# Performance work log

Measured on AMD Instinct MI355X. Metric: run time of the kernel, lower is better.

The kernel has to match this reference:

```python
import jax, jax.numpy as jnp
import numpy as np

N_NODES = 100000
N_EDGES = 1600000


def _mean_agg(x, src, dst, n):
    # mean over incoming neighbors: scatter-add gathered features, divide by degree
    agg = jax.ops.segment_sum(x[src], dst, num_segments=n)  # [N, d]
    deg = jax.ops.segment_sum(jnp.ones((src.shape[0],), x.dtype), dst, num_segments=n)
    return agg / jnp.maximum(deg, 1.0)[:, None]


def _sage_conv(x, src, dst, Wl, Wr, b):
    # PyG SAGEConv (aggr='mean', root_weight=True): lin_l(mean_agg) + lin_r(x) + bias
    n = x.shape[0]
    agg = _mean_agg(x, src, dst, n)
    return agg @ Wl + x @ Wr + b


def setup_inputs() -> dict:
    key = jax.random.key(0)
    ks = jax.random.split(key, 12)
    d_in, d_h, d_out = 128, 256, 47
    x = jax.random.normal(ks[0], (N_NODES, d_in), dtype=jnp.float32)
    src = jax.random.randint(ks[1], (N_EDGES,), 0, N_NODES, dtype=jnp.int32)
    dst = jax.random.randint(ks[2], (N_EDGES,), 0, N_NODES, dtype=jnp.int32)

    def glorot(k, shape):
        lim = 1.0 / np.sqrt(shape[0])
        return jax.random.uniform(k, shape, jnp.float32, -lim, lim)

    return {
        "x": x, "src": src, "dst": dst,
        "Wl0": glorot(ks[3], (d_in, d_h)), "Wr0": glorot(ks[4], (d_in, d_h)), "b0": jnp.zeros((d_h,), jnp.float32),
        "Wl1": glorot(ks[5], (d_h, d_h)), "Wr1": glorot(ks[6], (d_h, d_h)), "b1": jnp.zeros((d_h,), jnp.float32),
        "Wl2": glorot(ks[7], (d_h, d_out)), "Wr2": glorot(ks[8], (d_h, d_out)), "b2": jnp.zeros((d_out,), jnp.float32),
    }


def reference(x, src, dst, Wl0, Wr0, b0, Wl1, Wr1, b1, Wl2, Wr2, b2):
    # layer 1 + ReLU (dropout inactive at inference)
    h = jax.nn.relu(_sage_conv(x, src, dst, Wl0, Wr0, b0))
    # layer 2 + ReLU
    h = jax.nn.relu(_sage_conv(h, src, dst, Wl1, Wr1, b1))
    # output layer + log_softmax
    h = _sage_conv(h, src, dst, Wl2, Wr2, b2)
    return jax.nn.log_softmax(h, axis=-1)
```

## Files before the change

### kernel.cpp

```cpp
#include <hip/hip_runtime.h>
#include <stdint.h>

typedef unsigned int u32;
typedef unsigned short u16;

typedef __attribute__((ext_vector_type(4))) float f32x4;
typedef __attribute__((ext_vector_type(8))) __bf16 bf16x8;

#define NN 100000
#define NE 1600000
#define NSLICE 8
#define SLICE_NODES 12500

typedef __attribute__((address_space(1))) u32 ga_u32;
typedef __attribute__((address_space(3))) u32 ls_u32;

static __device__ __forceinline__ u32 f2bf_bits(float f){
  u32 u = __float_as_uint(f);
  return (u + 0x7fffu + ((u >> 16) & 1u)) >> 16;
}
static __device__ __forceinline__ float bf2f(u16 h){ return __uint_as_float(((u32)h) << 16); }

static __device__ __forceinline__ void gload16(const void* g, void* l){
  __builtin_amdgcn_global_load_lds((const ga_u32*)g, (ls_u32*)l, 16, 0, 0);
}

__global__ void k_hist(const int* __restrict__ dst, int* __restrict__ cnt){
  int e = blockIdx.x*256 + threadIdx.x;
  if (e < NE) atomicAdd(&cnt[dst[e]], 1);
}

__global__ void k_scan1(const int* __restrict__ cnt, int* __restrict__ excl, int* __restrict__ bsum){
  __shared__ int s[1024];
  int t = threadIdx.x;
  int i = blockIdx.x*1024 + t;
  int v = (i < NN) ? cnt[i] : 0;
  s[t] = v; __syncthreads();
  int acc = v;
  for (int off = 1; off < 1024; off <<= 1){
    int tmp = (t >= off) ? s[t-off] : 0;
    __syncthreads();
    acc += tmp; s[t] = acc;
    __syncthreads();
  }
  if (i < NN) excl[i] = acc - v;
  if (t == 1023) bsum[blockIdx.x] = acc;
}

__global__ void k_scan2(int* bsum, int nb){
  if (threadIdx.x == 0 && blockIdx.x == 0){
    int run = 0;
    for (int b = 0; b < nb; b++){ int t = bsum[b]; bsum[b] = run; run += t; }
  }
}

__global__ void k_scan3(const int* __restrict__ cnt, int* __restrict__ row_start,
                        const int* __restrict__ bsum, int* __restrict__ fill_ptr,
                        float* __restrict__ rdeg){
  int i = blockIdx.x*256 + threadIdx.x;
  if (i >= NN) return;
  int rs = row_start[i] + bsum[i >> 10];
  row_start[i] = rs;
  fill_ptr[i]  = rs;
  int c = cnt[i];
  rdeg[i] = 1.0f / (float)(c > 1 ? c : 1);
}

__global__ __launch_bounds__(256) void k_fill(const int* __restrict__ src,
    const int* __restrict__ dst, int* __restrict__ fill_ptr, int* __restrict__ ssrc){
  int slice = blockIdx.x & 7;
  int bin   = blockIdx.x >> 3;
  int nbin  = gridDim.x >> 3;
  int lo = slice * SLICE_NODES;
  int hi = lo + SLICE_NODES;
  for (int e = bin*256 + threadIdx.x; e < NE; e += nbin*256){
    int d = dst[e];
    if (d >= lo && d < hi){
      int pos = atomicAdd(&fill_ptr[d], 1);
      ssrc[pos] = src[e];
    }
  }
}

__global__ void k_wprep(const float* __restrict__ Wl0, const float* __restrict__ Wr0,
                        const float* __restrict__ Wl1, const float* __restrict__ Wr1,
                        const float* __restrict__ Wl2, const float* __restrict__ Wr2,
                        u16* __restrict__ W1t, u16* __restrict__ W2t, u16* __restrict__ W3t){
  int idx = blockIdx.x*256 + threadIdx.x;
  if (idx < 256*256){
    int n = idx >> 8, k = idx & 255;
    float v = (k < 128) ? Wl0[k*256 + n] : Wr0[(k-128)*256 + n];
    W1t[idx] = (u16)f2bf_bits(v);
  } else if (idx < 256*256 + 256*512){
    int j = idx - 256*256;
    int n = j >> 9, k = j & 511;
    float v = (k < 256) ? Wl1[k*256 + n] : Wr1[(k-256)*256 + n];
    W2t[j] = (u16)f2bf_bits(v);
  } else {
    int j = idx - (256*256 + 256*512);
    int n = j >> 8, k = j & 255;
    float v = 0.f;
    if (n < 47) v = Wl2[k*47 + n];
    else if (n >= 48 && n < 95) v = Wr2[k*47 + (n-48)];
    W3t[j] = (u16)f2bf_bits(v);
  }
}

__global__ void k_xconv(const float* __restrict__ x, u16* __restrict__ xb){
  int i = blockIdx.x*256 + threadIdx.x;
  if (i >= NN*128/4) return;
  const float4* xp = (const float4*)x;
  float4 v = xp[i];
  u32 lo = f2bf_bits(v.x) | (f2bf_bits(v.y) << 16);
  u32 hi = f2bf_bits(v.z) | (f2bf_bits(v.w) << 16);
  ((u32*)xb)[2*i]   = lo;
  ((u32*)xb)[2*i+1] = hi;
}

template<int F, int UN>
__global__ __launch_bounds__(256) void k_agg(const u16* __restrict__ feat,
    const int* __restrict__ row_start, const int* __restrict__ cnt,
    const float* __restrict__ rdeg, const int* __restrict__ ssrc,
    u16* __restrict__ out){
  constexpr int EPL = F/64;
  int i = blockIdx.x*4 + (threadIdx.x >> 6);
  if (i >= NN) return;
  int lane = threadIdx.x & 63;
  const u16* fp = feat + (size_t)lane*EPL;
  int beg = row_start[i], num = cnt[i];
  float a0=0.f, b0=0.f, a1=0.f, b1=0.f;
  int j = 0;
  for (; j + UN <= num; j += UN){
    u32 w0[UN], w1[UN];
    #pragma unroll
    for (int u = 0; u < UN; u++){
      const u16* q = fp + (size_t)ssrc[beg+j+u]*F;
      if constexpr (EPL == 4){ uint2 t2 = *(const uint2*)q; w0[u] = t2.x; w1[u] = t2.y; }
      else                   { w0[u] = *(const u32*)q; }
    }
    #pragma unroll
    for (int u = 0; u < UN; u++){
      a0 += __uint_as_float(w0[u] << 16); b0 += __uint_as_float(w0[u] & 0xffff0000u);
      if constexpr (EPL == 4){
        a1 += __uint_as_float(w1[u] << 16); b1 += __uint_as_float(w1[u] & 0xffff0000u);
      }
    }
  }
  for (; j + 2 <= num; j += 2){
    u32 w0[2], w1[2];
    #pragma unroll
    for (int u = 0; u < 2; u++){
      const u16* q = fp + (size_t)ssrc[beg+j+u]*F;
      if constexpr (EPL == 4){ uint2 t2 = *(const uint2*)q; w0[u] = t2.x; w1[u] = t2.y; }
      else                   { w0[u] = *(const u32*)q; }
    }
    #pragma unroll
    for (int u = 0; u < 2; u++){
      a0 += __uint_as_float(w0[u] << 16); b0 += __uint_as_float(w0[u] & 0xffff0000u);
      if constexpr (EPL == 4){
        a1 += __uint_as_float(w1[u] << 16); b1 += __uint_as_float(w1[u] & 0xffff0000u);
      }
    }
  }
  if (j < num){
    const u16* q = fp + (size_t)ssrc[beg+j]*F;
    if constexpr (EPL == 4){
      uint2 t2 = *(const uint2*)q;
      a0 += __uint_as_float(t2.x << 16); b0 += __uint_as_float(t2.x & 0xffff0000u);
      a1 += __uint_as_float(t2.y << 16); b1 += __uint_as_float(t2.y & 0xffff0000u);
    } else {
      u32 p = *(const u32*)q;
      a0 += __uint_as_float(p << 16); b0 += __uint_as_float(p & 0xffff0000u);
    }
  }
  float r = rdeg[i];
  if constexpr (EPL == 4){
    uint2 pk;
    pk.x = f2bf_bits(a0*r) | (f2bf_bits(b0*r) << 16);
    pk.y = f2bf_bits(a1*r) | (f2bf_bits(b1*r) << 16);
    *(uint2*)(out + (size_t)i*F + lane*4) = pk;
  } else {
    *(u32*)(out + (size_t)i*F + lane*2) = f2bf_bits(a0*r) | (f2bf_bits(b0*r) << 16);
  }
}

template<bool RELU>
__global__ __launch_bounds__(256) void k_gemm(
    const u16* __restrict__ A1, int K1, const u16* __restrict__ A2, int K2,
    const u16* __restrict__ Bt, const float* __restrict__ bias,
    u16* __restrict__ C, int ldc){
  __shared__ u16 As[128*64];
  __shared__ u16 Bs[128*64];
  const int M = NN;
  const int K = K1 + K2;
  const int gm = (M + 127) >> 7;
  int bm = blockIdx.x % gm, bn = blockIdx.x / gm;
  int tid = threadIdx.x;
  int lane = tid & 63, w = tid >> 6;
  int wm = w >> 1, wn = w & 1;
  int lr = lane & 15, l4 = lane >> 4;
  f32x4 acc[4][4] = {};
  const int nk = K >> 6;
  for (int kstep = 0; kstep < nk; kstep++){
    __syncthreads();
    #pragma unroll
    for (int q = 0; q < 4; q++){
      int L = q*4096 + tid*16;
      int row = L >> 7;
      int c16 = ((L >> 4) & 7) ^ (row & 7);
      int gk = (kstep << 6) + (c16 << 3);
      int grow = bm*128 + row; if (grow >= M) grow = M - 1;
      const u16* ga = (gk < K1) ? (A1 + (size_t)grow*K1 + gk)
                                : (A2 + (size_t)grow*K2 + (gk - K1));
      gload16(ga, (char*)As + L);
      int gcol = bn*128 + row;
      gload16(Bt + (size_t)gcol*K + gk, (char*)Bs + L);
    }
    __syncthreads();
    #pragma unroll
    for (int kk = 0; kk < 2; kk++){
      bf16x8 af[4], bf[4];
      #pragma unroll
      for (int fm = 0; fm < 4; fm++){
        int row = wm*64 + fm*16 + lr;
        int c16 = (kk << 2) + l4;
        af[fm] = *(const bf16x8*)((const char*)As + row*128 + ((c16 ^ (row&7)) << 4));
      }
      #pragma unroll
      for (int fn = 0; fn < 4; fn++){
        int row = wn*64 + fn*16 + lr;
        int c16 = (kk << 2) + l4;
        bf[fn] = *(const bf16x8*)((const char*)Bs + row*128 + ((c16 ^ (row&7)) << 4));
      }
      #pragma unroll
      for (int fm = 0; fm < 4; fm++)
        #pragma unroll
        for (int fn = 0; fn < 4; fn++)
          acc[fm][fn] = __builtin_amdgcn_mfma_f32_16x16x32_bf16(af[fm], bf[fn], acc[fm][fn], 0, 0, 0);
    }
  }
  #pragma unroll
  for (int fn = 0; fn < 4; fn++){
    int col = bn*128 + wn*64 + fn*16 + lr;
    float bv = bias ? bias[col] : 0.f;
    #pragma unroll
    for (int fm = 0; fm < 4; fm++){
      #pragma unroll
      for (int q = 0; q < 4; q++){
        int rowg = bm*128 + wm*64 + fm*16 + l4*4 + q;
        if (rowg < M){
          float v = acc[fm][fn][q] + bv;
          if (RELU) v = fmaxf(v, 0.f);
          C[(size_t)rowg*ldc + col] = (u16)f2bf_bits(v);
        }
      }
    }
  }
}

__global__ __launch_bounds__(256) void k_final(const u16* __restrict__ G,
    const int* __restrict__ row_start, const int* __restrict__ cnt,
    const float* __restrict__ rdeg, const int* __restrict__ ssrc,
    const float* __restrict__ b2, float* __restrict__ out){
  int i = blockIdx.x*8 + (threadIdx.x >> 5);
  if (i >= NN) return;
  int t = threadIdx.x & 31;
  int beg = row_start[i], num = cnt[i];
  const u16* gp = G + 2*t;
  float a = 0.f, b = 0.f;
  int j = 0;
  for (; j + 4 <= num; j += 4){
    u32 w[4];
    #pragma unroll
    for (int u = 0; u < 4; u++) w[u] = *(const u32*)(gp + (size_t)ssrc[beg+j+u]*128);
    #pragma unroll
    for (int u = 0; u < 4; u++){ a += __uint_as_float(w[u] << 16); b += __uint_as_float(w[u] & 0xffff0000u); }
  }
  for (; j < num; j++){
    u32 w = *(const u32*)(gp + (size_t)ssrc[beg+j]*128);
    a += __uint_as_float(w << 16); b += __uint_as_float(w & 0xffff0000u);
  }
  float r = rdeg[i];
  u32 rw = *(const u32*)(G + (size_t)i*128 + 48 + 2*t);
  int f0 = 2*t, f1 = 2*t + 1;
  float va = (f0 < 47) ? a*r + __uint_as_float(rw << 16)          + b2[f0] : -3.0e38f;
  float vb = (f1 < 47) ? b*r + __uint_as_float(rw & 0xffff0000u)  + b2[f1] : -3.0e38f;
  float m = fmaxf(va, vb);
  #pragma unroll
  for (int o = 16; o > 0; o >>= 1) m = fmaxf(m, __shfl_xor(m, o, 32));
  float e = 0.f;
  if (f0 < 47) e += expf(va - m);
  if (f1 < 47) e += expf(vb - m);
  float s = e;
  #pragma unroll
  for (int o = 16; o > 0; o >>= 1) s += __shfl_xor(s, o, 32);
  float ls = logf(s);
  if (f0 < 47) out[(size_t)i*47 + f0] = va - m - ls;
  if (f1 < 47) out[(size_t)i*47 + f1] = vb - m - ls;
}

extern "C" void kernel_launch(void* const* d_in, const int* in_sizes, int n_in,
                              void* d_out, int out_size, void* d_ws, size_t ws_size,
                              hipStream_t stream){
  const float* x   = (const float*)d_in[0];
  const int*   src = (const int*)d_in[1];
  const int*   dst = (const int*)d_in[2];
  const float* Wl0 = (const float*)d_in[3];
  const float* Wr0 = (const float*)d_in[4];
  const float* b0  = (const float*)d_in[5];
  const float* Wl1 = (const float*)d_in[6];
  const float* Wr1 = (const float*)d_in[7];
  const float* b1  = (const float*)d_in[8];
  const float* Wl2 = (const float*)d_in[9];
  const float* Wr2 = (const float*)d_in[10];
  const float* b2  = (const float*)d_in[11];
  float* out = (float*)d_out;

  char* p = (char*)d_ws;
  size_t off = 0;
  auto alloc = [&](size_t bytes)->char*{
    char* r = p + off; off += (bytes + 511) & ~((size_t)511); return r;
  };
  int*   cnt       = (int*)  alloc((size_t)NN*4);
  int*   row_start = (int*)  alloc((size_t)NN*4);
  int*   fill_ptr  = (int*)  alloc((size_t)NN*4);
  float* rdeg      = (float*)alloc((size_t)NN*4);
  int*   bsum      = (int*)  alloc(512);
  int*   ssrc      = (int*)  alloc((size_t)NE*4);
  u16*   W1t       = (u16*)  alloc((size_t)256*256*2);
  u16*   W2t       = (u16*)  alloc((size_t)256*512*2);
  u16*   W3t       = (u16*)  alloc((size_t)128*256*2);
  u16*   xb        = (u16*)  alloc((size_t)NN*128*2);
  u16*   agg1      = (u16*)  alloc((size_t)NN*128*2);
  u16*   h1        = (u16*)  alloc((size_t)NN*256*2);
  u16*   agg2      = (u16*)  alloc((size_t)NN*256*2);
  u16*   h2        = (u16*)  alloc((size_t)NN*256*2);
  u16*   G = xb;

  const int nb_scan = (NN + 1023) / 1024;

  hipMemsetAsync(cnt, 0, (size_t)NN*4, stream);
  k_hist <<<NE/256, 256, 0, stream>>>(dst, cnt);
  k_scan1<<<nb_scan, 1024, 0, stream>>>(cnt, row_start, bsum);
  k_scan2<<<1, 64, 0, stream>>>(bsum, nb_scan);
  k_scan3<<<(NN+255)/256, 256, 0, stream>>>(cnt, row_start, bsum, fill_ptr, rdeg);
  k_fill <<<8*784, 256, 0, stream>>>(src, dst, fill_ptr, ssrc);
  k_wprep<<<(256*256 + 256*512 + 128*256)/256, 256, 0, stream>>>(Wl0,Wr0,Wl1,Wr1,Wl2,Wr2,W1t,W2t,W3t);
  k_xconv<<<(NN*128/4 + 255)/256, 256, 0, stream>>>(x, xb);

  k_agg<128,16><<<(NN+3)/4, 256, 0, stream>>>(xb, row_start, cnt, rdeg, ssrc, agg1);
  k_gemm<true><<<782*2, 256, 0, stream>>>(agg1, 128, xb, 128, W1t, b0, h1, 256);

  k_agg<256,8><<<(NN+3)/4, 256, 0, stream>>>(h1, row_start, cnt, rdeg, ssrc, agg2);
  k_gemm<true><<<782*2, 256, 0, stream>>>(agg2, 256, h1, 256, W2t, b1, h2, 256);

  k_gemm<false><<<782, 256, 0, stream>>>(h2, 256, h2, 0, W3t, nullptr, G, 128);
  k_final<<<(NN+7)/8, 256, 0, stream>>>(G, row_start, cnt, rdeg, ssrc, b2, out);
}
```

Baseline: 669.2 us.

## Split wave across edges with 16-byte gathers and compact final-layer gather buffer

The aggregation kernel now has each lane load 8 bf16 features (16 bytes) per edge. The wave splits into subgroups that process different edges in parallel, and their partial sums are combined with cross-lane shuffles. This is meant to raise memory-level parallelism and cut per-edge latency for the gather-bound steps. The final-layer GEMM also writes the neighbor part and the root part into separate 64-wide arrays, so the last gather reads half-size rows. The cost is extra shuffle reductions and an added branch in the GEMM epilogue.

```diff
diff --git a/kernel.cpp b/kernel.cpp
--- a/kernel.cpp
+++ b/kernel.cpp
@@ -101,7 +101,7 @@
     int n = j >> 8, k = j & 255;
     float v = 0.f;
     if (n < 47) v = Wl2[k*47 + n];
-    else if (n >= 48 && n < 95) v = Wr2[k*47 + (n-48)];
+    else if (n >= 64 && n < 111) v = Wr2[k*47 + (n-64)];
     W3t[j] = (u16)f2bf_bits(v);
   }
 }
@@ -117,70 +117,59 @@
   ((u32*)xb)[2*i+1] = hi;
 }
 
+static __device__ __forceinline__ void acc8(float* a, uint4 w){
+  a[0] += __uint_as_float(w.x << 16); a[1] += __uint_as_float(w.x & 0xffff0000u);
+  a[2] += __uint_as_float(w.y << 16); a[3] += __uint_as_float(w.y & 0xffff0000u);
+  a[4] += __uint_as_float(w.z << 16); a[5] += __uint_as_float(w.z & 0xffff0000u);
+  a[6] += __uint_as_float(w.w << 16); a[7] += __uint_as_float(w.w & 0xffff0000u);
+}
+
 template<int F, int UN>
 __global__ __launch_bounds__(256) void k_agg(const u16* __restrict__ feat,
     const int* __restrict__ row_start, const int* __restrict__ cnt,
     const float* __restrict__ rdeg, const int* __restrict__ ssrc,
     u16* __restrict__ out){
-  constexpr int EPL = F/64;
+  constexpr int LPR = F/8;
+  constexpr int G   = 64/LPR;
   int i = blockIdx.x*4 + (threadIdx.x >> 6);
   if (i >= NN) return;
   int lane = threadIdx.x & 63;
-  const u16* fp = feat + (size_t)lane*EPL;
+  int lir  = lane & (LPR-1);
+  int sub  = lane >> (F == 256 ? 5 : 4);
+  const u16* base = feat + lir*8;
   int beg = row_start[i], num = cnt[i];
-  float a0=0.f, b0=0.f, a1=0.f, b1=0.f;
+  float a[8] = {0.f,0.f,0.f,0.f,0.f,0.f,0.f,0.f};
   int j = 0;
-  for (; j + UN <= num; j += UN){
-    u32 w0[UN], w1[UN];
-    #pragma unroll
-    for (int u = 0; u < UN; u++){
-      const u16* q = fp + (size_t)ssrc[beg+j+u]*F;
-      if constexpr (EPL == 4){ uint2 t2 = *(const uint2*)q; w0[u] = t2.x; w1[u] = t2.y; }
-      else                   { w0[u] = *(const u32*)q; }
-    }
-    #pragma unroll
-    for (int u = 0; u < UN; u++){
-      a0 += __uint_as_float(w0[u] << 16); b0 += __uint_as_float(w0[u] & 0xffff0000u);
-      if constexpr (EPL == 4){
-        a1 += __uint_as_float(w1[u] << 16); b1 += __uint_as_float(w1[u] & 0xffff0000u);
-      }
-    }
-  }
-  for (; j + 2 <= num; j += 2){
-    u32 w0[2], w1[2];
-    #pragma unroll
-    for (int u = 0; u < 2; u++){
-      const u16* q = fp + (size_t)ssrc[beg+j+u]*F;
-      if constexpr (EPL == 4){ uint2 t2 = *(const uint2*)q; w0[u] = t2.x; w1[u] = t2.y; }
-      else                   { w0[u] = *(const u32*)q; }
-    }
-    #pragma unroll
-    for (int u = 0; u < 2; u++){
-      a0 += __uint_as_float(w0[u] << 16); b0 += __uint_as_float(w0[u] & 0xffff0000u);
-      if constexpr (EPL == 4){
-        a1 += __uint_as_float(w1[u] << 16); b1 += __uint_as_float(w1[u] & 0xffff0000u);
-      }
-    }
-  }
-  if (j < num){
-    const u16* q = fp + (size_t)ssrc[beg+j]*F;
-    if constexpr (EPL == 4){
-      uint2 t2 = *(const uint2*)q;
-      a0 += __uint_as_float(t2.x << 16); b0 += __uint_as_float(t2.x & 0xffff0000u);
-      a1 += __uint_as_float(t2.y << 16); b1 += __uint_as_float(t2.y & 0xffff0000u);
-    } else {
-      u32 p = *(const u32*)q;
-      a0 += __uint_as_float(p << 16); b0 += __uint_as_float(p & 0xffff0000u);
-    }
-  }
-  float r = rdeg[i];
-  if constexpr (EPL == 4){
-    uint2 pk;
-    pk.x = f2bf_bits(a0*r) | (f2bf_bits(b0*r) << 16);
-    pk.y = f2bf_bits(a1*r) | (f2bf_bits(b1*r) << 16);
-    *(uint2*)(out + (size_t)i*F + lane*4) = pk;
-  } else {
-    *(u32*)(out + (size_t)i*F + lane*2) = f2bf_bits(a0*r) | (f2bf_bits(b0*r) << 16);
+  for (; j + G*UN <= num; j += G*UN){
+    uint4 w[UN];
+    #pragma unroll
+    for (int u = 0; u < UN; u++)
+      w[u] = *(const uint4*)(base + (size_t)ssrc[beg + j + u*G + sub]*F);
+    #pragma unroll
+    for (int u = 0; u < UN; u++) acc8(a, w[u]);
+  }
+  for (; j + G <= num; j += G){
+    uint4 w = *(const uint4*)(base + (size_t)ssrc[beg + j + sub]*F);
+    acc8(a, w);
+  }
+  int rem = num - j;
+  if (rem > 0){
+    int idx = ssrc[beg + j + (sub < rem ? sub : 0)];
+    uint4 w = *(const uint4*)(base + (size_t)idx*F);
+    if (sub < rem) acc8(a, w);
+  }
+  #pragma unroll
+  for (int k = 0; k < 8; k++)
+    for (int off = LPR; off < 64; off <<= 1)
+      a[k] += __shfl_xor(a[k], off, 64);
+  if (sub == 0){
+    float r = rdeg[i];
+    uint4 pk;
+    pk.x = f2bf_bits(a[0]*r) | (f2bf_bits(a[1]*r) << 16);
+    pk.y = f2bf_bits(a[2]*r) | (f2bf_bits(a[3]*r) << 16);
+    pk.z = f2bf_bits(a[4]*r) | (f2bf_bits(a[5]*r) << 16);
+    pk.w = f2bf_bits(a[6]*r) | (f2bf_bits(a[7]*r) << 16);
+    *(uint4*)(out + (size_t)i*F + lir*8) = pk;
   }
 }
 
@@ -188,7 +177,7 @@
 __global__ __launch_bounds__(256) void k_gemm(
     const u16* __restrict__ A1, int K1, const u16* __restrict__ A2, int K2,
     const u16* __restrict__ Bt, const float* __restrict__ bias,
-    u16* __restrict__ C, int ldc){
+    u16* __restrict__ C, int ldc, u16* __restrict__ C2){
   __shared__ u16 As[128*64];
   __shared__ u16 Bs[128*64];
   const int M = NN;
@@ -251,37 +240,42 @@
         if (rowg < M){
           float v = acc[fm][fn][q] + bv;
           if (RELU) v = fmaxf(v, 0.f);
-          C[(size_t)rowg*ldc + col] = (u16)f2bf_bits(v);
+          u16* cp;
+          if (C2 == nullptr) cp = C + (size_t)rowg*ldc + col;
+          else cp = (col < 64) ? C  + (size_t)rowg*64 + col
+                               : C2 + (size_t)rowg*64 + (col - 64);
+          *cp = (u16)f2bf_bits(v);
         }
       }
     }
   }
 }
 
-__global__ __launch_bounds__(256) void k_final(const u16* __restrict__ G,
-    const int* __restrict__ row_start, const int* __restrict__ cnt,
-    const float* __restrict__ rdeg, const int* __restrict__ ssrc,
-    const float* __restrict__ b2, float* __restrict__ out){
+__global__ __launch_bounds__(256) void k_final(const u16* __restrict__ Gl,
+    const u16* __restrict__ Gr, const int* __restrict__ row_start,
+    const int* __restrict__ cnt, const float* __restrict__ rdeg,
+    const int* __restrict__ ssrc, const float* __restrict__ b2,
+    float* __restrict__ out){
   int i = blockIdx.x*8 + (threadIdx.x >> 5);
   if (i >= NN) return;
   int t = threadIdx.x & 31;
   int beg = row_start[i], num = cnt[i];
-  const u16* gp = G + 2*t;
+  const u16* gp = Gl + 2*t;
   float a = 0.f, b = 0.f;
   int j = 0;
   for (; j + 4 <= num; j += 4){
     u32 w[4];
     #pragma unroll
-    for (int u = 0; u < 4; u++) w[u] = *(const u32*)(gp + (size_t)ssrc[beg+j+u]*128);
+    for (int u = 0; u < 4; u++) w[u] = *(const u32*)(gp + (size_t)ssrc[beg+j+u]*64);
     #pragma unroll
     for (int u = 0; u < 4; u++){ a += __uint_as_float(w[u] << 16); b += __uint_as_float(w[u] & 0xffff0000u); }
   }
   for (; j < num; j++){
-    u32 w = *(const u32*)(gp + (size_t)ssrc[beg+j]*128);
+    u32 w = *(const u32*)(gp + (size_t)ssrc[beg+j]*64);
     a += __uint_as_float(w << 16); b += __uint_as_float(w & 0xffff0000u);
   }
   float r = rdeg[i];
-  u32 rw = *(const u32*)(G + (size_t)i*128 + 48 + 2*t);
+  u32 rw = *(const u32*)(Gr + (size_t)i*64 + 2*t);
   int f0 = 2*t, f1 = 2*t + 1;
   float va = (f0 < 47) ? a*r + __uint_as_float(rw << 16)          + b2[f0] : -3.0e38f;
   float vb = (f1 < 47) ? b*r + __uint_as_float(rw & 0xffff0000u)  + b2[f1] : -3.0e38f;
@@ -335,7 +329,8 @@
   u16*   h1        = (u16*)  alloc((size_t)NN*256*2);
   u16*   agg2      = (u16*)  alloc((size_t)NN*256*2);
   u16*   h2        = (u16*)  alloc((size_t)NN*256*2);
-  u16*   G = xb;
+  u16*   Gl = xb;
+  u16*   Gr = xb + (size_t)NN*64;
 
   const int nb_scan = (NN + 1023) / 1024;
 
@@ -348,12 +343,12 @@
   k_wprep<<<(256*256 + 256*512 + 128*256)/256, 256, 0, stream>>>(Wl0,Wr0,Wl1,Wr1,Wl2,Wr2,W1t,W2t,W3t);
   k_xconv<<<(NN*128/4 + 255)/256, 256, 0, stream>>>(x, xb);
 
-  k_agg<128,16><<<(NN+3)/4, 256, 0, stream>>>(xb, row_start, cnt, rdeg, ssrc, agg1);
-  k_gemm<true><<<782*2, 256, 0, stream>>>(agg1, 128, xb, 128, W1t, b0, h1, 256);
-
-  k_agg<256,8><<<(NN+3)/4, 256, 0, stream>>>(h1, row_start, cnt, rdeg, ssrc, agg2);
-  k_gemm<true><<<782*2, 256, 0, stream>>>(agg2, 256, h1, 256, W2t, b1, h2, 256);
-
-  k_gemm<false><<<782, 256, 0, stream>>>(h2, 256, h2, 0, W3t, nullptr, G, 128);
-  k_final<<<(NN+7)/8, 256, 0, stream>>>(G, row_start, cnt, rdeg, ssrc, b2, out);
-}
+  k_agg<128,4><<<(NN+3)/4, 256, 0, stream>>>(xb, row_start, cnt, rdeg, ssrc, agg1);
+  k_gemm<true><<<782*2, 256, 0, stream>>>(agg1, 128, xb, 128, W1t, b0, h1, 256, nullptr);
+
+  k_agg<256,6><<<(NN+3)/4, 256, 0, stream>>>(h1, row_start, cnt, rdeg, ssrc, agg2);
+  k_gemm<true><<<782*2, 256, 0, stream>>>(agg2, 256, h1, 256, W2t, b1, h2, 256, nullptr);
+
+  k_gemm<false><<<782, 256, 0, stream>>>(h2, 256, h2, 0, W3t, nullptr, Gl, 64, Gr);
+  k_final<<<(NN+7)/8, 256, 0, stream>>>(Gl, Gr, row_start, cnt, rdeg, ssrc, b2, out);
+}
```

Measured after the change: 653.7 us. -2.3%, faster.
